# Kernel tuning notes

Hardware: AMD Instinct MI355X
Metric: run time of the kernel (lower is better)

The kernel has to match this reference:

```python
import jax, jax.numpy as jnp
import numpy as np

N_NODES = 50000
N_EDGES = 800000
IN_F = 191
H1, C1 = 16, 16   # conv1: heads=16, out=16, concat -> 256
H2, C2 = 8, 3     # conv2: heads=8, out=3, concat=False -> mean


def _glorot(key, shape):
    fan = shape[0] + shape[-1] if len(shape) == 2 else sum(shape)
    s = jnp.sqrt(6.0 / fan)
    return jax.random.uniform(key, shape, jnp.float32, -s, s)


def setup_inputs() -> dict:
    key = jax.random.key(0)
    ks = jax.random.split(key, 16)
    x = jax.random.normal(ks[0], (N_NODES, IN_F), jnp.float32)
    edge_index = jax.random.randint(ks[1], (2, N_EDGES), 0, N_NODES)
    edge_attr = jax.random.normal(ks[2], (N_EDGES, 1), jnp.float32)
    return {
        "x": x, "edge_index": edge_index, "edge_attr": edge_attr,
        "W1": _glorot(ks[3], (IN_F, H1 * C1)),
        "We1": _glorot(ks[4], (1, H1 * C1)),
        "a_src1": _glorot(ks[5], (H1, C1)),
        "a_dst1": _glorot(ks[6], (H1, C1)),
        "a_edge1": _glorot(ks[7], (H1, C1)),
        "b1": jnp.zeros((H1 * C1,), jnp.float32),
        "W2": _glorot(ks[8], (H1 * C1, H2 * C2)),
        "We2": _glorot(ks[9], (1, H2 * C2)),
        "a_src2": _glorot(ks[10], (H2, C2)),
        "a_dst2": _glorot(ks[11], (H2, C2)),
        "a_edge2": _glorot(ks[12], (H2, C2)),
        "b2": jnp.zeros((C2,), jnp.float32),
    }


def gat_conv(x, src, dst, edge_attr, W, We, a_src, a_dst, a_edge, bias, H, C, concat):
    # x: [N, F]; src/dst: [E'] (self loops already appended); edge_attr: [E', De]
    N = x.shape[0]
    xl = (x @ W).reshape(N, H, C)                       # [N,H,C]
    e = (edge_attr @ We).reshape(-1, H, C)              # [E',H,C]
    alpha_src = (xl * a_src).sum(-1)                    # [N,H]
    alpha_dst = (xl * a_dst).sum(-1)                    # [N,H]
    alpha_e = (e * a_edge).sum(-1)                      # [E',H]
    alpha = alpha_src[src] + alpha_dst[dst] + alpha_e   # [E',H]
    alpha = jax.nn.leaky_relu(alpha, 0.2)
    # softmax over incoming edges per destination node
    m = jax.ops.segment_max(alpha, dst, num_segments=N)
    alpha = jnp.exp(alpha - m[dst])
    den = jax.ops.segment_sum(alpha, dst, num_segments=N)
    alpha = alpha / (den[dst] + 1e-16)
    out = jax.ops.segment_sum(alpha[:, :, None] * xl[src], dst, num_segments=N)  # [N,H,C]
    if concat:
        return out.reshape(N, H * C) + bias
    return out.mean(axis=1) + bias


def reference(x, edge_index, edge_attr, W1, We1, a_src1, a_dst1, a_edge1, b1,
              W2, We2, a_src2, a_dst2, a_edge2, b2):
    N = x.shape[0]
    # add self loops (PyG default, edge_attr fill_value='mean')
    loop = jnp.arange(N)
    src = jnp.concatenate([edge_index[0], loop])
    dst = jnp.concatenate([edge_index[1], loop])
    ea_mean = edge_attr.mean(axis=0, keepdims=True)
    ea = jnp.concatenate([edge_attr, jnp.broadcast_to(ea_mean, (N, edge_attr.shape[1]))], axis=0)

    h = gat_conv(x, src, dst, ea, W1, We1, a_src1, a_dst1, a_edge1, b1, H1, C1, True)
    h = jax.nn.elu(h)
    h = gat_conv(h, src, dst, ea, W2, We2, a_src2, a_dst2, a_edge2, b2, H2, C2, False)
    h = jax.nn.elu(h)
    return h
```

## Files before the change

kernel.cpp:

```cpp
#include <hip/hip_runtime.h>
#include <math.h>
#include <stdint.h>

#define N_NODES 50000
#define N_EDGES 800000
#define N_TOT   850000
#define IN_F    191
#define F1      256
#define NH1     16
#define NC1     16
#define F2      24
#define NH2     8
#define NC2     3
#define KP      224
#define MPAD    50048
#define NCVT_X  (MPAD * 28)
#define NCVT_W  (F1 * 28)

typedef __attribute__((ext_vector_type(8))) short bf16x8;
typedef __attribute__((ext_vector_type(4))) float f32x4;

#define GLL16(g, s) __builtin_amdgcn_global_load_lds( \
    (const __attribute__((address_space(1))) void*)(g), \
    (__attribute__((address_space(3))) void*)(s), 16, 0, 0)

__device__ __forceinline__ float lrelu(float x) { return x > 0.f ? x : 0.2f * x; }

__device__ __forceinline__ uint16_t f2bf1(float f) {
    uint32_t u = __float_as_uint(f);
    return (uint16_t)((u + 0x7fffu + ((u >> 16) & 1u)) >> 16);
}
__device__ __forceinline__ uint16_t f2bf(float f, float* back) {
    uint32_t u = __float_as_uint(f);
    uint32_t r = (u + 0x7fffu + ((u >> 16) & 1u)) >> 16;
    *back = __uint_as_float(r << 16);
    return (uint16_t)r;
}
__device__ __forceinline__ void bf2f2(uint32_t u, float* lo, float* hi) {
    *lo = __uint_as_float(u << 16);
    *hi = __uint_as_float(u & 0xffff0000u);
}

__global__ void k_hist(const int* __restrict__ ei, int* counts) {
    int e = blockIdx.x * blockDim.x + threadIdx.x;
    if (e < N_EDGES) atomicAdd(&counts[ei[N_EDGES + e]], 1);
}

__global__ void k_easum(const float* __restrict__ ea, float* scalars) {
    __shared__ float wsums[4];
    int t = threadIdx.x;
    float v = 0.f;
    for (int e = blockIdx.x * 256 + t; e < N_EDGES; e += 256 * 256) v += ea[e];
    #pragma unroll
    for (int off = 32; off >= 1; off >>= 1) v += __shfl_xor(v, off);
    if ((t & 63) == 0) wsums[t >> 6] = v;
    __syncthreads();
    if (t == 0) atomicAdd(&scalars[25], wsums[0] + wsums[1] + wsums[2] + wsums[3]);
}

__global__ void k_wedot(const float* __restrict__ We1, const float* __restrict__ ae1,
                        const float* __restrict__ We2, const float* __restrict__ ae2,
                        float* scalars) {
    int t = threadIdx.x;
    if (t < NH1) {
        float s = 0.f;
        for (int c = 0; c < NC1; c++) s += We1[t * NC1 + c] * ae1[t * NC1 + c];
        scalars[1 + t] = s;
    } else if (t < NH1 + NH2) {
        int h = t - NH1;
        float s = 0.f;
        for (int c = 0; c < NC2; c++) s += We2[h * NC2 + c] * ae2[h * NC2 + c];
        scalars[17 + h] = s;
    } else if (t == 63) {
        scalars[0] = scalars[25] / (float)N_EDGES;
    }
}

__global__ __launch_bounds__(1024) void k_scan1(const int* __restrict__ counts,
                                                int* rowptr, int* bsums) {
    __shared__ int wsum[16];
    int t = threadIdx.x;
    int lane = t & 63, w = t >> 6;
    int i = blockIdx.x * 1024 + t;
    int v = (i < N_NODES) ? counts[i] + 1 : 0;
    int incl = v;
    #pragma unroll
    for (int off = 1; off < 64; off <<= 1) {
        int u = __shfl_up(incl, off);
        if (lane >= off) incl += u;
    }
    if (lane == 63) wsum[w] = incl;
    __syncthreads();
    int woff = 0;
    #pragma unroll
    for (int k = 0; k < 16; k++) woff += (k < w) ? wsum[k] : 0;
    if (i < N_NODES) rowptr[i] = woff + incl - v;
    if (t == 1023) bsums[blockIdx.x] = woff + incl;
}

__global__ __launch_bounds__(1024) void k_scan2(int* rowptr, int* cursor,
                                                const int* __restrict__ bsums) {
    __shared__ int off_s;
    int b = blockIdx.x, t = threadIdx.x;
    if (t == 0) {
        int o = 0;
        for (int k = 0; k < b; k++) o += bsums[k];
        off_s = o;
        if (b == 48) rowptr[N_NODES] = o + bsums[48];
    }
    __syncthreads();
    int i = b * 1024 + t;
    if (i < N_NODES) {
        int r = rowptr[i] + off_s;
        rowptr[i] = r;
        cursor[i] = r;
    }
}

__global__ void k_scatter(const int* __restrict__ ei, const float* __restrict__ ea,
                          const float* __restrict__ scalars, int* cursor,
                          int* csr_src, float* csr_ea) {
    int i = blockIdx.x * blockDim.x + threadIdx.x;
    if (i < N_EDGES) {
        int s = ei[i], d = ei[N_EDGES + i];
        int pos = atomicAdd(&cursor[d], 1);
        csr_src[pos] = s;
        csr_ea[pos] = ea[i];
    } else if (i < N_TOT) {
        int n = i - N_EDGES;
        int pos = atomicAdd(&cursor[n], 1);
        csr_src[pos] = n;
        csr_ea[pos] = scalars[0];
    }
}

__global__ void k_cvt(const float* __restrict__ x, const float* __restrict__ W1,
                      uint16_t* __restrict__ xh, uint16_t* __restrict__ xl,
                      uint16_t* __restrict__ wht, uint16_t* __restrict__ wlt) {
    int idx = blockIdx.x * 256 + threadIdx.x;
    if (idx < NCVT_X) {
        int row = idx / 28, kw = idx - row * 28;
        int k0 = kw * 8;
        uint16_t hv[8], lv[8];
        #pragma unroll
        for (int j = 0; j < 8; j++) {
            int k = k0 + j;
            float v = (row < N_NODES && k < IN_F) ? x[(size_t)row * IN_F + k] : 0.f;
            float hf;
            hv[j] = f2bf(v, &hf);
            lv[j] = f2bf1(v - hf);
        }
        *(uint4*)(xh + (size_t)row * KP + k0) = *(const uint4*)hv;
        *(uint4*)(xl + (size_t)row * KP + k0) = *(const uint4*)lv;
    } else if (idx < NCVT_X + NCVT_W) {
        int id2 = idx - NCVT_X;
        int col = id2 / 28, kw = id2 - col * 28;
        int k0 = kw * 8;
        uint16_t hv[8], lv[8];
        #pragma unroll
        for (int j = 0; j < 8; j++) {
            int k = k0 + j;
            float v = (k < IN_F) ? W1[(size_t)k * F1 + col] : 0.f;
            float hf;
            hv[j] = f2bf(v, &hf);
            lv[j] = f2bf1(v - hf);
        }
        *(uint4*)(wht + (size_t)col * KP + k0) = *(const uint4*)hv;
        *(uint4*)(wlt + (size_t)col * KP + k0) = *(const uint4*)lv;
    }
}

__global__ __launch_bounds__(256) void k_gemm1_mfma(const uint16_t* __restrict__ xh,
        const uint16_t* __restrict__ xl, const uint16_t* __restrict__ wht,
        const uint16_t* __restrict__ wlt, uint16_t* __restrict__ xl1b) {
    __shared__ uint16_t lds[4 * 8 * 64 * 8];
    const int t = threadIdx.x;
    const int l = t & 63, w = t >> 6;
    const int wm = w >> 1, wn = w & 1;
    const int m0 = blockIdx.x * 128;
    const int n0 = blockIdx.y * 128;
    const int lr = l & 15, lk = l >> 4;

    uint16_t* ldsAh = lds;
    uint16_t* ldsAl = lds + 8 * 64 * 8;
    uint16_t* ldsBh = lds + 2 * 8 * 64 * 8;
    uint16_t* ldsBl = lds + 3 * 8 * 64 * 8;

    f32x4 acc[4][4];
    #pragma unroll
    for (int i = 0; i < 4; i++)
        #pragma unroll
        for (int j = 0; j < 4; j++)
            acc[i][j] = (f32x4){0.f, 0.f, 0.f, 0.f};

    for (int ks = 0; ks < 7; ks++) {
        const int kb = ks * 32 + lk * 8;
        #pragma unroll
        for (int ii = 0; ii < 2; ii++) {
            const int f = 2 * w + ii;
            const uint16_t* sAh = xh  + (size_t)(m0 + f * 16 + lr) * KP + kb;
            const uint16_t* sAl = xl  + (size_t)(m0 + f * 16 + lr) * KP + kb;
            const uint16_t* sBh = wht + (size_t)(n0 + f * 16 + lr) * KP + kb;
            const uint16_t* sBl = wlt + (size_t)(n0 + f * 16 + lr) * KP + kb;
            GLL16(sAh, ldsAh + f * 512);
            GLL16(sAl, ldsAl + f * 512);
            GLL16(sBh, ldsBh + f * 512);
            GLL16(sBl, ldsBl + f * 512);
        }
        __syncthreads();
        bf16x8 ah[4], al[4];
        #pragma unroll
        for (int i = 0; i < 4; i++) {
            const int f = wm * 4 + i;
            ah[i] = *(const bf16x8*)(ldsAh + (f * 64 + l) * 8);
            al[i] = *(const bf16x8*)(ldsAl + (f * 64 + l) * 8);
        }
        #pragma unroll
        for (int j = 0; j < 4; j++) {
            const int g = wn * 4 + j;
            bf16x8 bh = *(const bf16x8*)(ldsBh + (g * 64 + l) * 8);
            bf16x8 bl = *(const bf16x8*)(ldsBl + (g * 64 + l) * 8);
            #pragma unroll
            for (int i = 0; i < 4; i++) {
                acc[i][j] = __builtin_amdgcn_mfma_f32_16x16x32_bf16(ah[i], bh, acc[i][j], 0, 0, 0);
                acc[i][j] = __builtin_amdgcn_mfma_f32_16x16x32_bf16(ah[i], bl, acc[i][j], 0, 0, 0);
                acc[i][j] = __builtin_amdgcn_mfma_f32_16x16x32_bf16(al[i], bh, acc[i][j], 0, 0, 0);
            }
        }
        __syncthreads();
    }
    #pragma unroll
    for (int i = 0; i < 4; i++) {
        const int gm_base = m0 + wm * 64 + i * 16 + lk * 4;
        #pragma unroll
        for (int r = 0; r < 4; r++) {
            const int gm = gm_base + r;
            if (gm < N_NODES) {
                #pragma unroll
                for (int j = 0; j < 4; j++) {
                    const int gn = n0 + wn * 64 + j * 16 + lr;
                    xl1b[(size_t)gm * F1 + gn] = f2bf1(acc[i][j][r]);
                }
            }
        }
    }
}

__global__ void k_alphas1(const uint16_t* __restrict__ xl1b, const float* __restrict__ a_src,
                          const float* __restrict__ a_dst,
                          float* __restrict__ asrc, float* __restrict__ adst) {
    int idx = blockIdx.x * blockDim.x + threadIdx.x;
    if (idx >= N_NODES * NH1) return;
    int h = idx & 15;
    const uint4* xp = (const uint4*)(xl1b + (size_t)idx * 16);
    uint4 u0 = xp[0], u1 = xp[1];
    uint32_t us[8] = {u0.x, u0.y, u0.z, u0.w, u1.x, u1.y, u1.z, u1.w};
    float as = 0.f, ad = 0.f;
    #pragma unroll
    for (int q = 0; q < 8; q++) {
        float lo, hi;
        bf2f2(us[q], &lo, &hi);
        as += lo * a_src[h * 16 + 2 * q] + hi * a_src[h * 16 + 2 * q + 1];
        ad += lo * a_dst[h * 16 + 2 * q] + hi * a_dst[h * 16 + 2 * q + 1];
    }
    asrc[idx] = as;
    adst[idx] = ad;
}

__global__ __launch_bounds__(256) void k_agg1(const int* __restrict__ rowptr,
        const int* __restrict__ csr_src, const float* __restrict__ csr_ea,
        const uint16_t* __restrict__ xl1b, const float* __restrict__ asrc,
        const float* __restrict__ adst, const float* __restrict__ scalars,
        const float* __restrict__ b1, uint16_t* __restrict__ h1b) {
    int node = blockIdx.x * 4 + (threadIdx.x >> 6);
    int lane = threadIdx.x & 63;
    int eg = lane >> 4, h = lane & 15;
    int r0 = rowptr[node], r1 = rowptr[node + 1];
    float ad = adst[node * 16 + h];
    float wd = scalars[1 + h];
    float den = 0.f;
    float acc[16];
    #pragma unroll
    for (int c = 0; c < 16; c++) acc[c] = 0.f;
    int j = r0 + eg;
    for (; j + 4 < r1; j += 8) {
        int s0 = csr_src[j], s1 = csr_src[j + 4];
        float e0 = csr_ea[j], e1 = csr_ea[j + 4];
        float p0 = asrc[s0 * 16 + h], p1 = asrc[s1 * 16 + h];
        const uint4* xp0 = (const uint4*)(xl1b + (size_t)s0 * F1 + h * 16);
        const uint4* xp1 = (const uint4*)(xl1b + (size_t)s1 * F1 + h * 16);
        uint4 u0a = xp0[0], u0b = xp0[1];
        uint4 u1a = xp1[0], u1b = xp1[1];
        float w0 = __expf(lrelu(p0 + ad + e0 * wd));
        float w1 = __expf(lrelu(p1 + ad + e1 * wd));
        den += w0 + w1;
        float lo, hi;
        bf2f2(u0a.x, &lo, &hi); acc[0] += w0 * lo;  acc[1] += w0 * hi;
        bf2f2(u0a.y, &lo, &hi); acc[2] += w0 * lo;  acc[3] += w0 * hi;
        bf2f2(u0a.z, &lo, &hi); acc[4] += w0 * lo;  acc[5] += w0 * hi;
        bf2f2(u0a.w, &lo, &hi); acc[6] += w0 * lo;  acc[7] += w0 * hi;
        bf2f2(u0b.x, &lo, &hi); acc[8] += w0 * lo;  acc[9] += w0 * hi;
        bf2f2(u0b.y, &lo, &hi); acc[10] += w0 * lo; acc[11] += w0 * hi;
        bf2f2(u0b.z, &lo, &hi); acc[12] += w0 * lo; acc[13] += w0 * hi;
        bf2f2(u0b.w, &lo, &hi); acc[14] += w0 * lo; acc[15] += w0 * hi;
        bf2f2(u1a.x, &lo, &hi); acc[0] += w1 * lo;  acc[1] += w1 * hi;
        bf2f2(u1a.y, &lo, &hi); acc[2] += w1 * lo;  acc[3] += w1 * hi;
        bf2f2(u1a.z, &lo, &hi); acc[4] += w1 * lo;  acc[5] += w1 * hi;
        bf2f2(u1a.w, &lo, &hi); acc[6] += w1 * lo;  acc[7] += w1 * hi;
        bf2f2(u1b.x, &lo, &hi); acc[8] += w1 * lo;  acc[9] += w1 * hi;
        bf2f2(u1b.y, &lo, &hi); acc[10] += w1 * lo; acc[11] += w1 * hi;
        bf2f2(u1b.z, &lo, &hi); acc[12] += w1 * lo; acc[13] += w1 * hi;
        bf2f2(u1b.w, &lo, &hi); acc[14] += w1 * lo; acc[15] += w1 * hi;
    }
    if (j < r1) {
        int s = csr_src[j];
        float a = lrelu(asrc[s * 16 + h] + ad + csr_ea[j] * wd);
        float wgt = __expf(a);
        den += wgt;
        const uint4* xp = (const uint4*)(xl1b + (size_t)s * F1 + h * 16);
        uint4 u0 = xp[0], u1 = xp[1];
        float lo, hi;
        bf2f2(u0.x, &lo, &hi); acc[0] += wgt * lo;  acc[1] += wgt * hi;
        bf2f2(u0.y, &lo, &hi); acc[2] += wgt * lo;  acc[3] += wgt * hi;
        bf2f2(u0.z, &lo, &hi); acc[4] += wgt * lo;  acc[5] += wgt * hi;
        bf2f2(u0.w, &lo, &hi); acc[6] += wgt * lo;  acc[7] += wgt * hi;
        bf2f2(u1.x, &lo, &hi); acc[8] += wgt * lo;  acc[9] += wgt * hi;
        bf2f2(u1.y, &lo, &hi); acc[10] += wgt * lo; acc[11] += wgt * hi;
        bf2f2(u1.z, &lo, &hi); acc[12] += wgt * lo; acc[13] += wgt * hi;
        bf2f2(u1.w, &lo, &hi); acc[14] += wgt * lo; acc[15] += wgt * hi;
    }
    den += __shfl_xor(den, 16);
    den += __shfl_xor(den, 32);
    float inv = 1.f / (den + 1e-16f);
    #pragma unroll
    for (int c = 0; c < 16; c++) {
        acc[c] += __shfl_xor(acc[c], 16);
        acc[c] += __shfl_xor(acc[c], 32);
    }
    if (eg == 0) {
        uint32_t pk[8];
        #pragma unroll
        for (int q = 0; q < 8; q++) {
            float v0 = acc[2 * q] * inv + b1[h * 16 + 2 * q];
            float v1 = acc[2 * q + 1] * inv + b1[h * 16 + 2 * q + 1];
            v0 = v0 > 0.f ? v0 : expm1f(v0);
            v1 = v1 > 0.f ? v1 : expm1f(v1);
            pk[q] = (uint32_t)f2bf1(v0) | ((uint32_t)f2bf1(v1) << 16);
        }
        uint4* op = (uint4*)(h1b + (size_t)node * F1 + h * 16);
        op[0] = make_uint4(pk[0], pk[1], pk[2], pk[3]);
        op[1] = make_uint4(pk[4], pk[5], pk[6], pk[7]);
    }
}

__global__ __launch_bounds__(256) void k_gemm2(const uint16_t* __restrict__ h1b,
                                               const float* __restrict__ W2,
                                               uint16_t* __restrict__ xl2b) {
    __shared__ float W2t[F2][260];
    int t = threadIdx.x;
    for (int i = t; i < 256 * F2; i += 256) {
        int k = i / F2, c = i - k * F2;
        W2t[c][k] = W2[i];
    }
    __syncthreads();
    int idx = blockIdx.x * 256 + t;
    if (idx >= N_NODES * F2) return;
    int n = idx / F2, col = idx - n * F2;
    const uint4* hp = (const uint4*)(h1b + (size_t)n * F1);
    float acc = 0.f;
    #pragma unroll 4
    for (int q = 0; q < 32; q++) {
        uint4 u = hp[q];
        const float4* wp = (const float4*)(&W2t[col][q * 8]);
        float4 w0 = wp[0], w1 = wp[1];
        float lo, hi;
        bf2f2(u.x, &lo, &hi); acc += lo * w0.x + hi * w0.y;
        bf2f2(u.y, &lo, &hi); acc += lo * w0.z + hi * w0.w;
        bf2f2(u.z, &lo, &hi); acc += lo * w1.x + hi * w1.y;
        bf2f2(u.w, &lo, &hi); acc += lo * w1.z + hi * w1.w;
    }
    int hh = col / 3, cc = col - hh * 3;
    xl2b[(size_t)n * 32 + hh * 4 + cc] = f2bf1(acc);
}

__global__ void k_xl2pad(uint16_t* __restrict__ xl2b) {
    int i = blockIdx.x * 256 + threadIdx.x;
    if (i < N_NODES * 8) xl2b[(size_t)i * 4 + 3] = 0;
}

__global__ void k_alphas2(const uint16_t* __restrict__ xl2b, const float* __restrict__ a_src,
                          const float* __restrict__ a_dst,
                          float* __restrict__ asrc, float* __restrict__ adst) {
    int idx = blockIdx.x * blockDim.x + threadIdx.x;
    if (idx >= N_NODES * NH2) return;
    int h = idx & 7;
    const uint2* xp = (const uint2*)(xl2b + (size_t)idx * 4);
    uint2 u = xp[0];
    float x0, x1, x2, dummy;
    bf2f2(u.x, &x0, &x1);
    bf2f2(u.y, &x2, &dummy);
    asrc[idx] = x0 * a_src[h * 3 + 0] + x1 * a_src[h * 3 + 1] + x2 * a_src[h * 3 + 2];
    adst[idx] = x0 * a_dst[h * 3 + 0] + x1 * a_dst[h * 3 + 1] + x2 * a_dst[h * 3 + 2];
}

__global__ __launch_bounds__(256) void k_agg2(const int* __restrict__ rowptr,
        const int* __restrict__ csr_src, const float* __restrict__ csr_ea,
        const uint16_t* __restrict__ xl2b, const float* __restrict__ asrc,
        const float* __restrict__ adst, const float* __restrict__ scalars,
        const float* __restrict__ b2, float* __restrict__ out) {
    int node = blockIdx.x * 4 + (threadIdx.x >> 6);
    int lane = threadIdx.x & 63;
    int eg = lane >> 3, h = lane & 7;
    int r0 = rowptr[node], r1 = rowptr[node + 1];
    float ad = adst[node * 8 + h];
    float wd = scalars[17 + h];
    float den = 0.f, a0 = 0.f, a1 = 0.f, a2 = 0.f;
    for (int j = r0 + eg; j < r1; j += 8) {
        int s = csr_src[j];
        float a = lrelu(asrc[s * 8 + h] + ad + csr_ea[j] * wd);
        float wgt = __expf(a);
        den += wgt;
        const uint2* xp = (const uint2*)(xl2b + ((size_t)s * 8 + h) * 4);
        uint2 u = xp[0];
        float x0, x1, x2, dummy;
        bf2f2(u.x, &x0, &x1);
        bf2f2(u.y, &x2, &dummy);
        a0 += wgt * x0;
        a1 += wgt * x1;
        a2 += wgt * x2;
    }
    den += __shfl_xor(den, 8); den += __shfl_xor(den, 16); den += __shfl_xor(den, 32);
    float inv = 1.f / (den + 1e-16f);
    a0 += __shfl_xor(a0, 8); a0 += __shfl_xor(a0, 16); a0 += __shfl_xor(a0, 32);
    a1 += __shfl_xor(a1, 8); a1 += __shfl_xor(a1, 16); a1 += __shfl_xor(a1, 32);
    a2 += __shfl_xor(a2, 8); a2 += __shfl_xor(a2, 16); a2 += __shfl_xor(a2, 32);
    a0 *= inv; a1 *= inv; a2 *= inv;
    a0 += __shfl_xor(a0, 1); a0 += __shfl_xor(a0, 2); a0 += __shfl_xor(a0, 4);
    a1 += __shfl_xor(a1, 1); a1 += __shfl_xor(a1, 2); a1 += __shfl_xor(a1, 4);
    a2 += __shfl_xor(a2, 1); a2 += __shfl_xor(a2, 2); a2 += __shfl_xor(a2, 4);
    if (lane == 0) {
        float v0 = a0 * 0.125f + b2[0];
        float v1 = a1 * 0.125f + b2[1];
        float v2 = a2 * 0.125f + b2[2];
        out[node * 3 + 0] = v0 > 0.f ? v0 : expm1f(v0);
        out[node * 3 + 1] = v1 > 0.f ? v1 : expm1f(v1);
        out[node * 3 + 2] = v2 > 0.f ? v2 : expm1f(v2);
    }
}

extern "C" void kernel_launch(void* const* d_in, const int* in_sizes, int n_in,
                              void* d_out, int out_size, void* d_ws, size_t ws_size,
                              hipStream_t stream) {
    const float* x       = (const float*)d_in[0];
    const int*   ei      = (const int*)d_in[1];
    const float* ea      = (const float*)d_in[2];
    const float* W1      = (const float*)d_in[3];
    const float* We1     = (const float*)d_in[4];
    const float* a_src1  = (const float*)d_in[5];
    const float* a_dst1  = (const float*)d_in[6];
    const float* a_edge1 = (const float*)d_in[7];
    const float* b1      = (const float*)d_in[8];
    const float* W2      = (const float*)d_in[9];
    const float* We2     = (const float*)d_in[10];
    const float* a_src2  = (const float*)d_in[11];
    const float* a_dst2  = (const float*)d_in[12];
    const float* a_edge2 = (const float*)d_in[13];
    const float* b2      = (const float*)d_in[14];
    float* out = (float*)d_out;

    char* ws = (char*)d_ws;
    size_t off = 0;
    auto alloc = [&](size_t nbytes) -> void* {
        void* p = ws + off;
        off = (off + nbytes + 255) & ~(size_t)255;
        return p;
    };
    uint16_t* xl1b = (uint16_t*)alloc((size_t)N_NODES * F1 * 2);
    uint16_t* h1b  = (uint16_t*)alloc((size_t)N_NODES * F1 * 2);
    float* asrc1   = (float*)alloc((size_t)N_NODES * NH1 * 4);
    float* adst1   = (float*)alloc((size_t)N_NODES * NH1 * 4);
    uint16_t* xl2b = (uint16_t*)alloc((size_t)N_NODES * 32 * 2);
    float* asrc2   = (float*)alloc((size_t)N_NODES * NH2 * 4);
    float* adst2   = (float*)alloc((size_t)N_NODES * NH2 * 4);
    int*   counts  = (int*)alloc((size_t)N_NODES * 4);
    int*   rowptr  = (int*)alloc((size_t)(N_NODES + 1) * 4);
    int*   cursor  = (int*)alloc((size_t)N_NODES * 4);
    int*   bsums   = (int*)alloc(64 * 4);
    int*   csr_src = (int*)alloc((size_t)N_TOT * 4);
    float* csr_ea  = (float*)alloc((size_t)N_TOT * 4);
    float* scalars = (float*)alloc(128);
    uint16_t* wht  = (uint16_t*)alloc((size_t)F1 * KP * 2);
    uint16_t* wlt  = (uint16_t*)alloc((size_t)F1 * KP * 2);
    uint16_t* xh   = (uint16_t*)alloc((size_t)MPAD * KP * 2);
    uint16_t* xlo  = (uint16_t*)alloc((size_t)MPAD * KP * 2);

    hipMemsetAsync(counts, 0, (size_t)N_NODES * 4, stream);
    hipMemsetAsync(scalars, 0, 128, stream);
    hipLaunchKernelGGL(k_hist, dim3((N_EDGES + 255) / 256), dim3(256), 0, stream,
                       ei, counts);
    hipLaunchKernelGGL(k_easum, dim3(256), dim3(256), 0, stream, ea, scalars);
    hipLaunchKernelGGL(k_wedot, dim3(1), dim3(64), 0, stream,
                       We1, a_edge1, We2, a_edge2, scalars);
    hipLaunchKernelGGL(k_scan1, dim3(49), dim3(1024), 0, stream, counts, rowptr, bsums);
    hipLaunchKernelGGL(k_scan2, dim3(49), dim3(1024), 0, stream, rowptr, cursor, bsums);
    hipLaunchKernelGGL(k_scatter, dim3((N_TOT + 255) / 256), dim3(256), 0, stream,
                       ei, ea, scalars, cursor, csr_src, csr_ea);
    hipLaunchKernelGGL(k_cvt, dim3((NCVT_X + NCVT_W + 255) / 256), dim3(256), 0, stream,
                       x, W1, xh, xlo, wht, wlt);
    hipLaunchKernelGGL(k_gemm1_mfma, dim3(MPAD / 128, 2), dim3(256), 0, stream,
                       xh, xlo, wht, wlt, xl1b);
    hipLaunchKernelGGL(k_alphas1, dim3((N_NODES * NH1 + 255) / 256), dim3(256), 0, stream,
                       xl1b, a_src1, a_dst1, asrc1, adst1);
    hipLaunchKernelGGL(k_agg1, dim3(N_NODES / 4), dim3(256), 0, stream,
                       rowptr, csr_src, csr_ea, xl1b, asrc1, adst1, scalars, b1, h1b);
    hipLaunchKernelGGL(k_xl2pad, dim3((N_NODES * 8 + 255) / 256), dim3(256), 0, stream,
                       xl2b);
    hipLaunchKernelGGL(k_gemm2, dim3((N_NODES * F2 + 255) / 256), dim3(256), 0, stream,
                       h1b, W2, xl2b);
    hipLaunchKernelGGL(k_alphas2, dim3((N_NODES * NH2 + 255) / 256), dim3(256), 0, stream,
                       xl2b, a_src2, a_dst2, asrc2, adst2);
    hipLaunchKernelGGL(k_agg2, dim3(N_NODES / 4), dim3(256), 0, stream,
                       rowptr, csr_src, csr_ea, xl2b, asrc2, adst2, scalars, b2, out);
}
```

Measured before the change: 326.4 us.

## Pack CSR arrays, shrink GEMM K padding, fuse layer-2 projection and alphas, simplify agg1

Several changes at once. The separate src and edge-attribute CSR arrays become one interleaved uint2 array, so each edge needs one load. The GEMM1 K padding drops from 224 to 192, which cuts one MFMA k-step and reduces conversion traffic. The layer-2 pad, GEMM and alpha kernels are merged into one kernel computing three outputs per thread, which removes two launches and the round trip through xl2b. The 2-way unrolled edge loop in agg1 is replaced by a simple single-edge loop, which may reduce memory-level parallelism in that gather-bound kernel.

Result: no change. 327.8 us (+0.4%).

```diff
diff --git a/kernel.cpp b/kernel.cpp
--- a/kernel.cpp
+++ b/kernel.cpp
@@ -12,10 +12,10 @@
 #define F2      24
 #define NH2     8
 #define NC2     3
-#define KP      224
+#define KP      192
 #define MPAD    50048
-#define NCVT_X  (MPAD * 28)
-#define NCVT_W  (F1 * 28)
+#define NCVT_X  (MPAD * 24)
+#define NCVT_W  (F1 * 24)
 
 typedef __attribute__((ext_vector_type(8))) short bf16x8;
 typedef __attribute__((ext_vector_type(4))) float f32x4;
@@ -119,18 +119,16 @@
 
 __global__ void k_scatter(const int* __restrict__ ei, const float* __restrict__ ea,
                           const float* __restrict__ scalars, int* cursor,
-                          int* csr_src, float* csr_ea) {
+                          uint2* __restrict__ csr) {
     int i = blockIdx.x * blockDim.x + threadIdx.x;
     if (i < N_EDGES) {
         int s = ei[i], d = ei[N_EDGES + i];
         int pos = atomicAdd(&cursor[d], 1);
-        csr_src[pos] = s;
-        csr_ea[pos] = ea[i];
+        csr[pos] = make_uint2((uint32_t)s, __float_as_uint(ea[i]));
     } else if (i < N_TOT) {
         int n = i - N_EDGES;
         int pos = atomicAdd(&cursor[n], 1);
-        csr_src[pos] = n;
-        csr_ea[pos] = scalars[0];
+        csr[pos] = make_uint2((uint32_t)n, __float_as_uint(scalars[0]));
     }
 }
 
@@ -139,7 +137,7 @@
                       uint16_t* __restrict__ wht, uint16_t* __restrict__ wlt) {
     int idx = blockIdx.x * 256 + threadIdx.x;
     if (idx < NCVT_X) {
-        int row = idx / 28, kw = idx - row * 28;
+        int row = idx / 24, kw = idx - row * 24;
         int k0 = kw * 8;
         uint16_t hv[8], lv[8];
         #pragma unroll
@@ -154,7 +152,7 @@
         *(uint4*)(xl + (size_t)row * KP + k0) = *(const uint4*)lv;
     } else if (idx < NCVT_X + NCVT_W) {
         int id2 = idx - NCVT_X;
-        int col = id2 / 28, kw = id2 - col * 28;
+        int col = id2 / 24, kw = id2 - col * 24;
         int k0 = kw * 8;
         uint16_t hv[8], lv[8];
         #pragma unroll
@@ -193,7 +191,7 @@
         for (int j = 0; j < 4; j++)
             acc[i][j] = (f32x4){0.f, 0.f, 0.f, 0.f};
 
-    for (int ks = 0; ks < 7; ks++) {
+    for (int ks = 0; ks < 6; ks++) {
         const int kb = ks * 32 + lk * 8;
         #pragma unroll
         for (int ii = 0; ii < 2; ii++) {
@@ -268,7 +266,7 @@
 }
 
 __global__ __launch_bounds__(256) void k_agg1(const int* __restrict__ rowptr,
-        const int* __restrict__ csr_src, const float* __restrict__ csr_ea,
+        const uint2* __restrict__ csr,
         const uint16_t* __restrict__ xl1b, const float* __restrict__ asrc,
         const float* __restrict__ adst, const float* __restrict__ scalars,
         const float* __restrict__ b1, uint16_t* __restrict__ h1b) {
@@ -282,39 +280,10 @@
     float acc[16];
     #pragma unroll
     for (int c = 0; c < 16; c++) acc[c] = 0.f;
-    int j = r0 + eg;
-    for (; j + 4 < r1; j += 8) {
-        int s0 = csr_src[j], s1 = csr_src[j + 4];
-        float e0 = csr_ea[j], e1 = csr_ea[j + 4];
-        float p0 = asrc[s0 * 16 + h], p1 = asrc[s1 * 16 + h];
-        const uint4* xp0 = (const uint4*)(xl1b + (size_t)s0 * F1 + h * 16);
-        const uint4* xp1 = (const uint4*)(xl1b + (size_t)s1 * F1 + h * 16);
-        uint4 u0a = xp0[0], u0b = xp0[1];
-        uint4 u1a = xp1[0], u1b = xp1[1];
-        float w0 = __expf(lrelu(p0 + ad + e0 * wd));
-        float w1 = __expf(lrelu(p1 + ad + e1 * wd));
-        den += w0 + w1;
-        float lo, hi;
-        bf2f2(u0a.x, &lo, &hi); acc[0] += w0 * lo;  acc[1] += w0 * hi;
-        bf2f2(u0a.y, &lo, &hi); acc[2] += w0 * lo;  acc[3] += w0 * hi;
-        bf2f2(u0a.z, &lo, &hi); acc[4] += w0 * lo;  acc[5] += w0 * hi;
-        bf2f2(u0a.w, &lo, &hi); acc[6] += w0 * lo;  acc[7] += w0 * hi;
-        bf2f2(u0b.x, &lo, &hi); acc[8] += w0 * lo;  acc[9] += w0 * hi;
-        bf2f2(u0b.y, &lo, &hi); acc[10] += w0 * lo; acc[11] += w0 * hi;
-        bf2f2(u0b.z, &lo, &hi); acc[12] += w0 * lo; acc[13] += w0 * hi;
-        bf2f2(u0b.w, &lo, &hi); acc[14] += w0 * lo; acc[15] += w0 * hi;
-        bf2f2(u1a.x, &lo, &hi); acc[0] += w1 * lo;  acc[1] += w1 * hi;
-        bf2f2(u1a.y, &lo, &hi); acc[2] += w1 * lo;  acc[3] += w1 * hi;
-        bf2f2(u1a.z, &lo, &hi); acc[4] += w1 * lo;  acc[5] += w1 * hi;
-        bf2f2(u1a.w, &lo, &hi); acc[6] += w1 * lo;  acc[7] += w1 * hi;
-        bf2f2(u1b.x, &lo, &hi); acc[8] += w1 * lo;  acc[9] += w1 * hi;
-        bf2f2(u1b.y, &lo, &hi); acc[10] += w1 * lo; acc[11] += w1 * hi;
-        bf2f2(u1b.z, &lo, &hi); acc[12] += w1 * lo; acc[13] += w1 * hi;
-        bf2f2(u1b.w, &lo, &hi); acc[14] += w1 * lo; acc[15] += w1 * hi;
-    }
-    if (j < r1) {
-        int s = csr_src[j];
-        float a = lrelu(asrc[s * 16 + h] + ad + csr_ea[j] * wd);
+    for (int j = r0 + eg; j < r1; j += 4) {
+        uint2 pk = csr[j];
+        int s = (int)pk.x;
+        float a = lrelu(asrc[s * 16 + h] + ad + __uint_as_float(pk.y) * wd);
         float wgt = __expf(a);
         den += wgt;
         const uint4* xp = (const uint4*)(xl1b + (size_t)s * F1 + h * 16);
@@ -353,58 +322,49 @@
     }
 }
 
-__global__ __launch_bounds__(256) void k_gemm2(const uint16_t* __restrict__ h1b,
-                                               const float* __restrict__ W2,
-                                               uint16_t* __restrict__ xl2b) {
-    __shared__ float W2t[F2][260];
+__global__ __launch_bounds__(256) void k_layer2(const uint16_t* __restrict__ h1b,
+        const float* __restrict__ W2, const float* __restrict__ a_src,
+        const float* __restrict__ a_dst, uint16_t* __restrict__ xl2b,
+        float* __restrict__ asrc, float* __restrict__ adst) {
+    __shared__ float W2s[F2][258];
     int t = threadIdx.x;
     for (int i = t; i < 256 * F2; i += 256) {
         int k = i / F2, c = i - k * F2;
-        W2t[c][k] = W2[i];
+        W2s[c][k] = W2[i];
     }
     __syncthreads();
     int idx = blockIdx.x * 256 + t;
-    if (idx >= N_NODES * F2) return;
-    int n = idx / F2, col = idx - n * F2;
+    if (idx >= N_NODES * NH2) return;
+    int n = idx >> 3, h = idx & 7;
+    int c0 = h * 3;
     const uint4* hp = (const uint4*)(h1b + (size_t)n * F1);
-    float acc = 0.f;
+    float a0 = 0.f, a1 = 0.f, a2 = 0.f;
     #pragma unroll 4
     for (int q = 0; q < 32; q++) {
         uint4 u = hp[q];
-        const float4* wp = (const float4*)(&W2t[col][q * 8]);
-        float4 w0 = wp[0], w1 = wp[1];
-        float lo, hi;
-        bf2f2(u.x, &lo, &hi); acc += lo * w0.x + hi * w0.y;
-        bf2f2(u.y, &lo, &hi); acc += lo * w0.z + hi * w0.w;
-        bf2f2(u.z, &lo, &hi); acc += lo * w1.x + hi * w1.y;
-        bf2f2(u.w, &lo, &hi); acc += lo * w1.z + hi * w1.w;
-    }
-    int hh = col / 3, cc = col - hh * 3;
-    xl2b[(size_t)n * 32 + hh * 4 + cc] = f2bf1(acc);
-}
-
-__global__ void k_xl2pad(uint16_t* __restrict__ xl2b) {
-    int i = blockIdx.x * 256 + threadIdx.x;
-    if (i < N_NODES * 8) xl2b[(size_t)i * 4 + 3] = 0;
-}
-
-__global__ void k_alphas2(const uint16_t* __restrict__ xl2b, const float* __restrict__ a_src,
-                          const float* __restrict__ a_dst,
-                          float* __restrict__ asrc, float* __restrict__ adst) {
-    int idx = blockIdx.x * blockDim.x + threadIdx.x;
-    if (idx >= N_NODES * NH2) return;
-    int h = idx & 7;
-    const uint2* xp = (const uint2*)(xl2b + (size_t)idx * 4);
-    uint2 u = xp[0];
-    float x0, x1, x2, dummy;
-    bf2f2(u.x, &x0, &x1);
-    bf2f2(u.y, &x2, &dummy);
-    asrc[idx] = x0 * a_src[h * 3 + 0] + x1 * a_src[h * 3 + 1] + x2 * a_src[h * 3 + 2];
-    adst[idx] = x0 * a_dst[h * 3 + 0] + x1 * a_dst[h * 3 + 1] + x2 * a_dst[h * 3 + 2];
+        float f[8];
+        bf2f2(u.x, &f[0], &f[1]);
+        bf2f2(u.y, &f[2], &f[3]);
+        bf2f2(u.z, &f[4], &f[5]);
+        bf2f2(u.w, &f[6], &f[7]);
+        #pragma unroll
+        for (int j = 0; j < 8; j++) {
+            int k = q * 8 + j;
+            a0 += f[j] * W2s[c0][k];
+            a1 += f[j] * W2s[c0 + 1][k];
+            a2 += f[j] * W2s[c0 + 2][k];
+        }
+    }
+    uint2 pk;
+    pk.x = (uint32_t)f2bf1(a0) | ((uint32_t)f2bf1(a1) << 16);
+    pk.y = (uint32_t)f2bf1(a2);
+    *(uint2*)(xl2b + (size_t)idx * 4) = pk;
+    asrc[idx] = a0 * a_src[h * 3 + 0] + a1 * a_src[h * 3 + 1] + a2 * a_src[h * 3 + 2];
+    adst[idx] = a0 * a_dst[h * 3 + 0] + a1 * a_dst[h * 3 + 1] + a2 * a_dst[h * 3 + 2];
 }
 
 __global__ __launch_bounds__(256) void k_agg2(const int* __restrict__ rowptr,
-        const int* __restrict__ csr_src, const float* __restrict__ csr_ea,
+        const uint2* __restrict__ csr,
         const uint16_t* __restrict__ xl2b, const float* __restrict__ asrc,
         const float* __restrict__ adst, const float* __restrict__ scalars,
         const float* __restrict__ b2, float* __restrict__ out) {
@@ -416,8 +376,9 @@
     float wd = scalars[17 + h];
     float den = 0.f, a0 = 0.f, a1 = 0.f, a2 = 0.f;
     for (int j = r0 + eg; j < r1; j += 8) {
-        int s = csr_src[j];
-        float a = lrelu(asrc[s * 8 + h] + ad + csr_ea[j] * wd);
+        uint2 pk = csr[j];
+        int s = (int)pk.x;
+        float a = lrelu(asrc[s * 8 + h] + ad + __uint_as_float(pk.y) * wd);
         float wgt = __expf(a);
         den += wgt;
         const uint2* xp = (const uint2*)(xl2b + ((size_t)s * 8 + h) * 4);
@@ -486,8 +447,7 @@
     int*   rowptr  = (int*)alloc((size_t)(N_NODES + 1) * 4);
     int*   cursor  = (int*)alloc((size_t)N_NODES * 4);
     int*   bsums   = (int*)alloc(64 * 4);
-    int*   csr_src = (int*)alloc((size_t)N_TOT * 4);
-    float* csr_ea  = (float*)alloc((size_t)N_TOT * 4);
+    uint2* csr     = (uint2*)alloc((size_t)N_TOT * 8);
     float* scalars = (float*)alloc(128);
     uint16_t* wht  = (uint16_t*)alloc((size_t)F1 * KP * 2);
     uint16_t* wlt  = (uint16_t*)alloc((size_t)F1 * KP * 2);
@@ -504,7 +464,7 @@
     hipLaunchKernelGGL(k_scan1, dim3(49), dim3(1024), 0, stream, counts, rowptr, bsums);
     hipLaunchKernelGGL(k_scan2, dim3(49), dim3(1024), 0, stream, rowptr, cursor, bsums);
     hipLaunchKernelGGL(k_scatter, dim3((N_TOT + 255) / 256), dim3(256), 0, stream,
-                       ei, ea, scalars, cursor, csr_src, csr_ea);
+                       ei, ea, scalars, cursor, csr);
     hipLaunchKernelGGL(k_cvt, dim3((NCVT_X + NCVT_W + 255) / 256), dim3(256), 0, stream,
                        x, W1, xh, xlo, wht, wlt);
     hipLaunchKernelGGL(k_gemm1_mfma, dim3(MPAD / 128, 2), dim3(256), 0, stream,
@@ -512,13 +472,9 @@
     hipLaunchKernelGGL(k_alphas1, dim3((N_NODES * NH1 + 255) / 256), dim3(256), 0, stream,
                        xl1b, a_src1, a_dst1, asrc1, adst1);
     hipLaunchKernelGGL(k_agg1, dim3(N_NODES / 4), dim3(256), 0, stream,
-                       rowptr, csr_src, csr_ea, xl1b, asrc1, adst1, scalars, b1, h1b);
-    hipLaunchKernelGGL(k_xl2pad, dim3((N_NODES * 8 + 255) / 256), dim3(256), 0, stream,
-                       xl2b);
-    hipLaunchKernelGGL(k_gemm2, dim3((N_NODES * F2 + 255) / 256), dim3(256), 0, stream,
-                       h1b, W2, xl2b);
-    hipLaunchKernelGGL(k_alphas2, dim3((N_NODES * NH2 + 255) / 256), dim3(256), 0, stream,
-                       xl2b, a_src2, a_dst2, asrc2, adst2);
+                       rowptr, csr, xl1b, asrc1, adst1, scalars, b1, h1b);
+    hipLaunchKernelGGL(k_layer2, dim3((N_NODES * NH2 + 255) / 256), dim3(256), 0, stream,
+                       h1b, W2, a_src2, a_dst2, xl2b, asrc2, adst2);
     hipLaunchKernelGGL(k_agg2, dim3(N_NODES / 4), dim3(256), 0, stream,
-                       rowptr, csr_src, csr_ea, xl2b, asrc2, adst2, scalars, b2, out);
-}
+                       rowptr, csr, xl2b, asrc2, adst2, scalars, b2, out);
+}
```
